# Optimization experiments

Measured on AMD Instinct MI355X. Metric: run time of the kernel, lower is better.

## Reference

```python
import jax, jax.numpy as jnp
import numpy as np

N_NODES = 1000
NODE_DIM = 40
SEQ_LEN = 12
IN_FEAT = 32
HID = 64
LAYERS = 3
GDEP = 2
TOPK = 20
TANH_ALPHA = 3.0
PROP_ALPHA = 0.05
LN_EPS = 1e-5


def setup_inputs() -> dict:
    key = jax.random.key(0)
    ks = jax.random.split(key, 20)
    s = 0.1  # weight init scale
    B = 64
    return {
        "x": jax.random.normal(ks[0], (B, N_NODES, SEQ_LEN, IN_FEAT), jnp.float32),
        # graph constructor params
        "emb1": jax.random.normal(ks[1], (N_NODES, NODE_DIM), jnp.float32) * s,
        "emb2": jax.random.normal(ks[2], (N_NODES, NODE_DIM), jnp.float32) * s,
        "lin1_w": jax.random.normal(ks[3], (NODE_DIM, NODE_DIM), jnp.float32) * s,
        "lin1_b": jnp.zeros((NODE_DIM,), jnp.float32),
        "lin2_w": jax.random.normal(ks[4], (NODE_DIM, NODE_DIM), jnp.float32) * s,
        "lin2_b": jnp.zeros((NODE_DIM,), jnp.float32),
        # LSTM (pytorch gate order i,f,g,o)
        "Wih": jax.random.normal(ks[5], (4 * HID, IN_FEAT), jnp.float32) * s,
        "Whh": jax.random.normal(ks[6], (4 * HID, HID), jnp.float32) * s,
        "bih": jnp.zeros((4 * HID,), jnp.float32),
        "bhh": jnp.zeros((4 * HID,), jnp.float32),
        # per-layer linear 64 -> seq_length
        "lin_w": jax.random.normal(ks[7], (LAYERS, SEQ_LEN, HID), jnp.float32) * s,
        "lin_b": jnp.zeros((LAYERS, SEQ_LEN), jnp.float32),
        # mixprop 1: (gdep+1)*12 -> 32
        "mp1_w": jax.random.normal(ks[8], (LAYERS, 32, (GDEP + 1) * SEQ_LEN), jnp.float32) * s,
        "mp1_b": jnp.zeros((LAYERS, 32), jnp.float32),
        # mixprop 2: (gdep+1)*32 -> node_dim
        "mp2_w": jax.random.normal(ks[9], (LAYERS, NODE_DIM, (GDEP + 1) * 32), jnp.float32) * s,
        "mp2_b": jnp.zeros((LAYERS, NODE_DIM), jnp.float32),
        # layernorm affine over (node_dim, N)
        "gamma": jnp.ones((LAYERS, NODE_DIM, N_NODES), jnp.float32),
        "beta": jnp.zeros((LAYERS, NODE_DIM, N_NODES), jnp.float32),
    }


def _graph_constructor(emb1, emb2, lin1_w, lin1_b, lin2_w, lin2_b):
    m1 = jnp.tanh(TANH_ALPHA * (emb1 @ lin1_w.T + lin1_b))
    m2 = jnp.tanh(TANH_ALPHA * (emb2 @ lin2_w.T + lin2_b))
    a = jax.nn.relu(jnp.tanh(TANH_ALPHA * (m1 @ m2.T - m2 @ m1.T)))
    _, idx = jax.lax.top_k(a, TOPK)  # keep top-k neighbors per row
    mask = jnp.zeros_like(a).at[jnp.arange(a.shape[0])[:, None], idx].set(1.0)
    return a * mask


def _lstm_last(x, Wih, Whh, bih, bhh):
    # x: (B, T, IN_FEAT) -> last hidden state (B, HID)
    B = x.shape[0]
    h0 = jnp.zeros((B, HID), x.dtype)
    c0 = jnp.zeros((B, HID), x.dtype)

    def step(carry, xt):
        h, c = carry
        g = xt @ Wih.T + h @ Whh.T + bih + bhh
        i, f, gg, o = jnp.split(g, 4, axis=-1)
        c = jax.nn.sigmoid(f) * c + jax.nn.sigmoid(i) * jnp.tanh(gg)
        h = jax.nn.sigmoid(o) * jnp.tanh(c)
        return (h, c), None

    (h, _), _ = jax.lax.scan(step, (h0, c0), jnp.swapaxes(x, 0, 1))
    return h


def _mixprop(h, adj_norm, w, b):
    # h: (B, C, N); adj_norm: (N, N) row-normalized (adj + I)
    x0 = h
    outs = [h]
    for _ in range(GDEP):
        h = PROP_ALPHA * x0 + (1.0 - PROP_ALPHA) * jnp.einsum('bcw,vw->bcv', h, adj_norm)
        outs.append(h)
    ho = jnp.concatenate(outs, axis=1)  # (B, C*(GDEP+1), N)
    return jnp.einsum('bcn,oc->bon', ho, w) + b[None, :, None]


def _layernorm(h, gamma, beta):
    # normalize over (C, N) dims
    mu = jnp.mean(h, axis=(1, 2), keepdims=True)
    var = jnp.var(h, axis=(1, 2), keepdims=True)
    return (h - mu) * jax.lax.rsqrt(var + LN_EPS) * gamma[None] + beta[None]


def reference(x, emb1, emb2, lin1_w, lin1_b, lin2_w, lin2_b,
              Wih, Whh, bih, bhh, lin_w, lin_b,
              mp1_w, mp1_b, mp2_w, mp2_b, gamma, beta):
    B, N, T, F = x.shape
    adj = _graph_constructor(emb1, emb2, lin1_w, lin1_b, lin2_w, lin2_b)
    adj = adj + jnp.eye(N, dtype=adj.dtype)
    adj_norm = adj / jnp.sum(adj, axis=1, keepdims=True)

    out = _lstm_last(x.reshape(B * N, T, F), Wih, Whh, bih, bhh)  # (B*N, 64)

    h = None
    for j in range(LAYERS):
        hj = out @ lin_w[j].T + lin_b[j]                # (B*N, 12)
        hj = hj.reshape(B, N, SEQ_LEN).transpose(0, 2, 1)  # (B, 12, N)
        hj = jax.nn.relu(_mixprop(hj, adj_norm, mp1_w[j], mp1_b[j]))
        # dropout is identity in eval mode
        hj = _mixprop(hj, adj_norm, mp2_w[j], mp2_b[j])  # (B, node_dim, N)
        h = _layernorm(hj, gamma[j], beta[j])

    return h.transpose(0, 2, 1).reshape(B, N * NODE_DIM)
```

## Files before the change

kernel.cpp:

```cpp
#include <hip/hip_runtime.h>


typedef unsigned short u16;
typedef __attribute__((ext_vector_type(8))) short bf16x8;
typedef __attribute__((ext_vector_type(4))) float fx4;

#define NB 64
#define NNODE 1000
#define TT 12
#define FF 32
#define HH 64
#define DD 40
#define TOPK_ 20
#define EPR 21

__device__ __forceinline__ float rcp_f(float x) { return __builtin_amdgcn_rcpf(x); }
__device__ __forceinline__ float tanh_f(float x) {
  return fmaf(-2.0f, rcp_f(__expf(2.0f * x) + 1.0f), 1.0f);
}
__device__ __forceinline__ unsigned int cvt_pk(float lo, float hi) {
  unsigned int r;
  asm("v_cvt_pk_bf16_f32 %0, %1, %2" : "=v"(r) : "v"(lo), "v"(hi));
  return r;
}
__device__ __forceinline__ bf16x8 cvt8(const float* p) {
  union { unsigned int u[4]; bf16x8 v; } r;
  #pragma unroll
  for (int e = 0; e < 4; e++) r.u[e] = cvt_pk(p[2 * e], p[2 * e + 1]);
  return r.v;
}
__device__ __forceinline__ bf16x8 cvt8v(float4 a, float4 b) {
  union { unsigned int u[4]; bf16x8 v; } r;
  r.u[0] = cvt_pk(a.x, a.y); r.u[1] = cvt_pk(a.z, a.w);
  r.u[2] = cvt_pk(b.x, b.y); r.u[3] = cvt_pk(b.z, b.w);
  return r.v;
}

__global__ void k_m1m2(const float* __restrict__ emb1, const float* __restrict__ emb2,
                       const float* __restrict__ w1, const float* __restrict__ b1,
                       const float* __restrict__ w2, const float* __restrict__ b2,
                       float* __restrict__ m1, float* __restrict__ m2) {
  int id = blockIdx.x * 256 + threadIdx.x;
  if (id >= 2 * NNODE * DD) return;
  int sel = id / (NNODE * DD);
  int r = id % (NNODE * DD);
  int i = r / DD, o = r % DD;
  const float* emb = sel ? emb2 : emb1;
  const float* w = sel ? w2 : w1;
  const float* bb = sel ? b2 : b1;
  float s = bb[o];
  for (int k = 0; k < DD; k++) s = fmaf(emb[i * DD + k], w[o * DD + k], s);
  (sel ? m2 : m1)[r] = tanh_f(3.0f * s);
}

__global__ void k_adj(const float* __restrict__ m1, const float* __restrict__ m2,
                      int2* __restrict__ pae) {
  int v = blockIdx.x, tid = threadIdx.x;
  __shared__ float arow[NNODE];
  __shared__ float m1v[DD], m2v[DD];
  if (tid < DD) { m1v[tid] = m1[v * DD + tid]; m2v[tid] = m2[v * DD + tid]; }
  __syncthreads();
  for (int w = tid; w < NNODE; w += 256) {
    float d1 = 0.f, d2 = 0.f;
    #pragma unroll 8
    for (int k = 0; k < DD; k++) {
      d1 = fmaf(m1v[k], m2[w * DD + k], d1);
      d2 = fmaf(m2v[k], m1[w * DD + k], d2);
    }
    arow[w] = fmaxf(tanh_f(3.0f * (d1 - d2)), 0.0f);
  }
  __syncthreads();
  if (tid >= 64) return;
  int l = tid;
  float rv[16];
  #pragma unroll
  for (int q = 0; q < 16; q++) {
    int idx = q * 64 + l;
    rv[q] = (idx < NNODE) ? arow[idx] : -2.f;
  }
  float rs = 1.f;
  float myv = 0.f; int myi = 0;
  #pragma unroll
  for (int sel = 0; sel < TOPK_; sel++) {
    float bv = rv[0]; int bi = l;
    #pragma unroll
    for (int q = 1; q < 16; q++) {
      int idx = q * 64 + l;
      if (rv[q] > bv) { bv = rv[q]; bi = idx; }
    }
    #pragma unroll
    for (int off = 1; off < 64; off <<= 1) {
      float ov = __shfl_xor(bv, off); int oi = __shfl_xor(bi, off);
      if (ov > bv || (ov == bv && oi < bi)) { bv = ov; bi = oi; }
    }
    rs += bv;
    if (l == sel + 1) { myv = bv; myi = bi; }
    #pragma unroll
    for (int q = 0; q < 16; q++)
      if (q * 64 + l == bi) rv[q] = -2.f;
  }
  float inv = rcp_f(rs);
  if (l == 0)          pae[v * EPR] = make_int2(v, __float_as_int(inv));
  else if (l <= TOPK_) pae[v * EPR + l] = make_int2(myi, __float_as_int(myv * inv));
}

__global__ __launch_bounds__(256, 2)
void k_lstm(const float* __restrict__ x, const float* __restrict__ Wih,
            const float* __restrict__ Whh, const float* __restrict__ bih,
            const float* __restrict__ bhh, const float* __restrict__ wt,
            float* __restrict__ hj) {
  __shared__ __align__(16) u16 whf[2 * 16 * 64 * 8];
  __shared__ __align__(16) u16 hsh[4][16][64];
  __shared__ float lwsh[12 * 64];
  __shared__ float lbsh[12];
  int tid = threadIdx.x, wave = tid >> 6, lane = tid & 63;
  int arow = lane & 15, kg = lane >> 4;

  for (int cc = tid; cc < 2 * 16 * 64; cc += 256) {
    int l = cc & 63, t16 = cc >> 6, ks = t16 >> 4, nt = t16 & 15;
    int row = (nt >> 2) * 64 + (l & 15) * 4 + (nt & 3);
    *(bf16x8*)&whf[cc * 8] = cvt8(Whh + row * 64 + ks * 32 + (l >> 4) * 8);
  }
  for (int i = tid; i < 768; i += 256) { int s = i >> 6, j = i & 63; lwsh[i] = wt[j * 12 + s]; }
  if (tid < 12) lbsh[tid] = wt[768 + tid];
  __syncthreads();

  bf16x8 wi[16];
  float biasv[16];
  #pragma unroll
  for (int nt = 0; nt < 16; nt++) {
    int row = (nt >> 2) * 64 + arow * 4 + (nt & 3);
    wi[nt] = cvt8(Wih + row * 32 + kg * 8);
    biasv[nt] = bih[row] + bhh[row];
  }

  int seq_base = blockIdx.x * 64 + wave * 16;
  const float* xb = x + (size_t)(seq_base + arow) * (TT * FF) + kg * 8;
  float cst[16];
  #pragma unroll
  for (int q = 0; q < 16; q++) cst[q] = 0.f;

  float4 xf0 = *(const float4*)(xb);
  float4 xf1 = *(const float4*)(xb + 4);

  auto STEP = [&](int t, bool first, float (&hq)[16]) {
    unsigned int zo = 0;
    asm volatile("" : "+v"(zo));
    bf16x8 xa = cvt8v(xf0, xf1);
    if (t < TT - 1) {
      xf0 = *(const float4*)(xb + (t + 1) * FF);
      xf1 = *(const float4*)(xb + (t + 1) * FF + 4);
    }
    fx4 acc[16];
    #pragma unroll
    for (int nt = 0; nt < 16; nt++)
      acc[nt] = (fx4){biasv[nt], biasv[nt], biasv[nt], biasv[nt]};
    #pragma unroll
    for (int nt = 0; nt < 16; nt++)
      acc[nt] = __builtin_amdgcn_mfma_f32_16x16x32_bf16(xa, wi[nt], acc[nt], 0, 0, 0);
    if (!first) {
      asm volatile("" ::: "memory");
      bf16x8 ha0 = *(const bf16x8*)&hsh[wave][arow][kg * 8];
      bf16x8 ha1 = *(const bf16x8*)&hsh[wave][arow][32 + kg * 8];
      asm volatile("" ::: "memory");
      #pragma unroll
      for (int nt = 0; nt < 16; nt++) {
        bf16x8 wb = *(const bf16x8*)&whf[(nt * 64 + lane) * 8 + zo];
        acc[nt] = __builtin_amdgcn_mfma_f32_16x16x32_bf16(ha0, wb, acc[nt], 0, 0, 0);
      }
      #pragma unroll
      for (int nt = 0; nt < 16; nt++) {
        bf16x8 wb = *(const bf16x8*)&whf[((16 + nt) * 64 + lane) * 8 + zo];
        acc[nt] = __builtin_amdgcn_mfma_f32_16x16x32_bf16(ha1, wb, acc[nt], 0, 0, 0);
      }
    }
    #pragma unroll
    for (int i = 0; i < 4; i++) {
      #pragma unroll
      for (int njt = 0; njt < 4; njt++) {
        float iv = acc[njt][i], fv = acc[njt + 4][i];
        float gv = acc[njt + 8][i], ov = acc[njt + 12][i];
        float cpv = cst[i * 4 + njt];
        float ei = __expf(-iv), ef = __expf(-fv);
        float eg = __expf(2.0f * gv), eo = __expf(-ov);
        float A = 1.0f + ef;
        float B = (1.0f + ei) * (eg + 1.0f);
        float c = fmaf(cpv, B, (eg - 1.0f) * A) * rcp_f(A * B);
        cst[i * 4 + njt] = c;
        float ec = __expf(2.0f * c);
        hq[i * 4 + njt] = (ec - 1.0f) * rcp_f((ec + 1.0f) * (1.0f + eo));
      }
    }
  };

  #pragma unroll 1
  for (int t = 0; t < TT - 1; t++) {
    float hq[16];
    STEP(t, t == 0, hq);
    #pragma unroll
    for (int i = 0; i < 4; i++) {
      unsigned int p0 = cvt_pk(hq[i * 4 + 0], hq[i * 4 + 1]);
      unsigned int p1 = cvt_pk(hq[i * 4 + 2], hq[i * 4 + 3]);
      *(uint2*)&hsh[wave][kg * 4 + i][arow * 4] = make_uint2(p0, p1);
    }
  }
  float hq[16];
  STEP(TT - 1, false, hq);

  #pragma unroll
  for (int i = 0; i < 4; i++) {
    float a[12];
    #pragma unroll
    for (int s = 0; s < 12; s++) a[s] = 0.f;
    #pragma unroll
    for (int njt = 0; njt < 4; njt++) {
      float hv = hq[i * 4 + njt];
      #pragma unroll
      for (int s = 0; s < 12; s++)
        a[s] = fmaf(hv, lwsh[s * 64 + arow * 4 + njt], a[s]);
    }
    #pragma unroll
    for (int off = 1; off < 16; off <<= 1) {
      #pragma unroll
      for (int s = 0; s < 12; s++) a[s] += __shfl_xor(a[s], off);
    }
    float outv = a[0];
    #pragma unroll
    for (int s = 1; s < 12; s++) outv = (arow == s) ? a[s] : outv;
    if (arow < 12) {
      int gseq = seq_base + kg * 4 + i;
      int bb = gseq / 1000, nn = gseq - bb * 1000;
      hj[(size_t)(bb * 12 + arow) * NNODE + nn] = outv + lbsh[arow];
    }
  }
}

__global__ void k_prep(const float* __restrict__ lw, const float* __restrict__ lb,
                       const float* __restrict__ w1, const float* __restrict__ b1,
                       const float* __restrict__ w2, const float* __restrict__ b2,
                       float* __restrict__ wt) {
  int tid = threadIdx.x;
  for (int i = tid; i < 768; i += 256) { int k = i / 12, s = i % 12; wt[i] = lw[s * 64 + k]; }
  if (tid < 12) wt[768 + tid] = lb[tid];
  for (int i = tid; i < 1152; i += 256) { int c = i / 32, o = i % 32; wt[784 + i] = w1[o * 36 + c]; }
  if (tid < 32) wt[1936 + tid] = b1[tid];
  for (int i = tid; i < 3840; i += 256) { int c = i / 40, o = i % 40; wt[1968 + i] = w2[o * 96 + c]; }
  if (tid < 40) wt[5808 + tid] = b2[tid];
}

__global__ void k_prop(const float* __restrict__ hin, const int2* __restrict__ pae,
                       float* __restrict__ ho, int C) {
  int blk = blockIdx.x;
  int b = blk / C, c = blk % C;
  __shared__ float r0[NNODE], r1[NNODE];
  int tid = threadIdx.x;
  const float* src = hin + (size_t)(b * C + c) * NNODE;
  float* dst = ho + (size_t)(b * 3 * C) * NNODE;
  for (int n = tid; n < NNODE; n += 256) {
    float vv = src[n]; r0[n] = vv; dst[(size_t)c * NNODE + n] = vv;
  }
  __syncthreads();
  for (int n = tid; n < NNODE; n += 256) {
    const int2* pa = pae + n * EPR;
    float s = 0.f;
    #pragma unroll
    for (int e = 0; e < EPR; e++) { int2 p = pa[e]; s = fmaf(__int_as_float(p.y), r0[p.x], s); }
    float h1 = 0.05f * r0[n] + 0.95f * s;
    r1[n] = h1; dst[(size_t)(C + c) * NNODE + n] = h1;
  }
  __syncthreads();
  for (int n = tid; n < NNODE; n += 256) {
    const int2* pa = pae + n * EPR;
    float s = 0.f;
    #pragma unroll
    for (int e = 0; e < EPR; e++) { int2 p = pa[e]; s = fmaf(__int_as_float(p.y), r1[p.x], s); }
    dst[(size_t)(2 * C + c) * NNODE + n] = 0.05f * r0[n] + 0.95f * s;
  }
}

template <int CIN, int COUT>
__global__ void k_proj(const float* __restrict__ hin, const float* __restrict__ wt,
                       const float* __restrict__ bb, float* __restrict__ out, int relu) {
  int id = blockIdx.x * 256 + threadIdx.x;
  int b = id / NNODE, n = id % NNODE;
  float acc[COUT];
  #pragma unroll
  for (int o = 0; o < COUT; o++) acc[o] = bb[o];
  for (int c = 0; c < CIN; c++) {
    float hv = hin[(size_t)(b * CIN + c) * NNODE + n];
    #pragma unroll
    for (int o = 0; o < COUT; o++) acc[o] = fmaf(hv, wt[c * COUT + o], acc[o]);
  }
  #pragma unroll
  for (int o = 0; o < COUT; o++) {
    float vv = acc[o];
    if (relu) vv = fmaxf(vv, 0.f);
    out[(size_t)(b * COUT + o) * NNODE + n] = vv;
  }
}

__global__ void k_lnstat(const float* __restrict__ hj2, float* __restrict__ stat) {
  int b = blockIdx.x, tid = threadIdx.x, lane = tid & 63, wave = tid >> 6;
  const float* p = hj2 + (size_t)b * DD * NNODE;
  float s = 0.f, q = 0.f;
  for (int i = tid; i < DD * NNODE; i += 256) { float vv = p[i]; s += vv; q = fmaf(vv, vv, q); }
  for (int off = 32; off; off >>= 1) { s += __shfl_down(s, off); q += __shfl_down(q, off); }
  __shared__ float ss[4], sq[4];
  if (lane == 0) { ss[wave] = s; sq[wave] = q; }
  __syncthreads();
  if (tid == 0) {
    const float invN = 1.0f / (float)(DD * NNODE);
    float S = ss[0] + ss[1] + ss[2] + ss[3];
    float Q = sq[0] + sq[1] + sq[2] + sq[3];
    float mu = S * invN;
    float var = Q * invN - mu * mu;
    stat[2 * b] = mu; stat[2 * b + 1] = __builtin_amdgcn_rsqf(var + 1e-5f);
  }
}

__global__ void k_lnapply(const float* __restrict__ hj2, const float* __restrict__ stat,
                          const float* __restrict__ gamma, const float* __restrict__ beta,
                          float* __restrict__ out) {
  int id = blockIdx.x * 256 + threadIdx.x;
  int b = id / NNODE, n = id % NNODE;
  float mu = stat[2 * b], rstd = stat[2 * b + 1];
  size_t obase = (size_t)b * (NNODE * DD) + (size_t)n * DD;
  #pragma unroll
  for (int d0 = 0; d0 < DD / 4; d0++) {
    float tt[4];
    #pragma unroll
    for (int q = 0; q < 4; q++) {
      int d = d0 * 4 + q;
      float h0 = hj2[(size_t)(b * DD + d) * NNODE + n];
      tt[q] = (h0 - mu) * rstd * gamma[d * NNODE + n] + beta[d * NNODE + n];
    }
    *(float4*)(out + obase + d0 * 4) = (float4){tt[0], tt[1], tt[2], tt[3]};
  }
}

#define OFF_M1   0
#define OFF_M2   40000
#define OFF_PAE  80000
#define OFF_HJ   4218000
#define OFF_HO1  4986000
#define OFF_O1   7290000
#define OFF_HO2  122000
#define OFF_HJ2  9338000
#define OFF_STAT 11898000
#define OFF_WT   11898128

extern "C" void kernel_launch(void* const* d_in, const int* in_sizes, int n_in,
                              void* d_out, int out_size, void* d_ws, size_t ws_size,
                              hipStream_t stream) {
  (void)in_sizes; (void)n_in; (void)out_size; (void)ws_size;
  const float* x     = (const float*)d_in[0];
  const float* emb1  = (const float*)d_in[1];
  const float* emb2  = (const float*)d_in[2];
  const float* l1w   = (const float*)d_in[3];
  const float* l1b   = (const float*)d_in[4];
  const float* l2w   = (const float*)d_in[5];
  const float* l2b   = (const float*)d_in[6];
  const float* Wih   = (const float*)d_in[7];
  const float* Whh   = (const float*)d_in[8];
  const float* bih   = (const float*)d_in[9];
  const float* bhh   = (const float*)d_in[10];
  const float* lin_w = (const float*)d_in[11];
  const float* lin_b = (const float*)d_in[12];
  const float* mp1w  = (const float*)d_in[13];
  const float* mp1b  = (const float*)d_in[14];
  const float* mp2w  = (const float*)d_in[15];
  const float* mp2b  = (const float*)d_in[16];
  const float* gamma = (const float*)d_in[17];
  const float* beta  = (const float*)d_in[18];

  float* ws   = (float*)d_ws;
  float* m1   = ws + OFF_M1;
  float* m2   = ws + OFF_M2;
  int2*  pae  = (int2*)(ws + OFF_PAE);
  float* hj   = ws + OFF_HJ;
  float* ho1  = ws + OFF_HO1;
  float* o1   = ws + OFF_O1;
  float* ho2  = ws + OFF_HO2;
  float* hj2  = ws + OFF_HJ2;
  float* stat = ws + OFF_STAT;
  float* wt   = ws + OFF_WT;

  k_m1m2<<<dim3(313), dim3(256), 0, stream>>>(emb1, emb2, l1w, l1b, l2w, l2b, m1, m2);
  k_prep<<<dim3(1), dim3(256), 0, stream>>>(lin_w + 1536, lin_b + 24, mp1w + 2304, mp1b + 64,
                                            mp2w + 7680, mp2b + 80, wt);
  k_adj<<<dim3(NNODE), dim3(256), 0, stream>>>(m1, m2, pae);
  k_lstm<<<dim3(1000), dim3(256), 0, stream>>>(x, Wih, Whh, bih, bhh, wt, hj);
  k_prop<<<dim3(64 * 12), dim3(256), 0, stream>>>(hj, pae, ho1, 12);
  k_proj<36, 32><<<dim3(250), dim3(256), 0, stream>>>(ho1, wt + 784, wt + 1936, o1, 1);
  k_prop<<<dim3(64 * 32), dim3(256), 0, stream>>>(o1, pae, ho2, 32);
  k_proj<96, 40><<<dim3(250), dim3(256), 0, stream>>>(ho2, wt + 1968, wt + 5808, hj2, 0);
  k_lnstat<<<dim3(NB), dim3(256), 0, stream>>>(hj2, stat);
  k_lnapply<<<dim3(250), dim3(256), 0, stream>>>(hj2, stat, gamma + 80000, beta + 80000,
                                                 (float*)d_out);
}
```

Measured before the change: 307.3 us.

## Vectorize loads, pad edge list to pairs, fold prep into m1m2, widen lnstat

Folds the weight-transpose prep kernel into an extra block of k_m1m2, which removes one launch. Uses float4 loads in the m1/m2 and adjacency dot products. Pads each node's edge list to 22 entries with a zero-weight dummy so k_prop can read edges as int4 pairs. Runs the layernorm stats with 1024 threads and float4 loads. The HO2 workspace offset is shifted to make room for the larger edge table, and the dummy edge adds a little work per node.

```diff
diff --git a/kernel.cpp b/kernel.cpp
--- a/kernel.cpp
+++ b/kernel.cpp
@@ -12,7 +12,7 @@
 #define HH 64
 #define DD 40
 #define TOPK_ 20
-#define EPR 21
+#define EPR2 22
 
 __device__ __forceinline__ float rcp_f(float x) { return __builtin_amdgcn_rcpf(x); }
 __device__ __forceinline__ float tanh_f(float x) {
@@ -39,17 +39,35 @@
 __global__ void k_m1m2(const float* __restrict__ emb1, const float* __restrict__ emb2,
                        const float* __restrict__ w1, const float* __restrict__ b1,
                        const float* __restrict__ w2, const float* __restrict__ b2,
-                       float* __restrict__ m1, float* __restrict__ m2) {
-  int id = blockIdx.x * 256 + threadIdx.x;
+                       float* __restrict__ m1, float* __restrict__ m2,
+                       const float* __restrict__ lw, const float* __restrict__ lb,
+                       const float* __restrict__ p1w, const float* __restrict__ p1b,
+                       const float* __restrict__ p2w, const float* __restrict__ p2b,
+                       float* __restrict__ wt) {
+  int tid = threadIdx.x;
+  if (blockIdx.x == 313) {
+    for (int i = tid; i < 768; i += 256) { int k = i / 12, s = i % 12; wt[i] = lw[s * 64 + k]; }
+    if (tid < 12) wt[768 + tid] = lb[tid];
+    for (int i = tid; i < 1152; i += 256) { int c = i / 32, o = i % 32; wt[784 + i] = p1w[o * 36 + c]; }
+    if (tid < 32) wt[1936 + tid] = p1b[tid];
+    for (int i = tid; i < 3840; i += 256) { int c = i / 40, o = i % 40; wt[1968 + i] = p2w[o * 96 + c]; }
+    if (tid < 40) wt[5808 + tid] = p2b[tid];
+    return;
+  }
+  int id = blockIdx.x * 256 + tid;
   if (id >= 2 * NNODE * DD) return;
   int sel = id / (NNODE * DD);
   int r = id % (NNODE * DD);
   int i = r / DD, o = r % DD;
-  const float* emb = sel ? emb2 : emb1;
-  const float* w = sel ? w2 : w1;
-  const float* bb = sel ? b2 : b1;
-  float s = bb[o];
-  for (int k = 0; k < DD; k++) s = fmaf(emb[i * DD + k], w[o * DD + k], s);
+  const float4* emb = (const float4*)((sel ? emb2 : emb1) + i * DD);
+  const float4* w = (const float4*)((sel ? w2 : w1) + o * DD);
+  float s = (sel ? b2 : b1)[o];
+  #pragma unroll
+  for (int k4 = 0; k4 < DD / 4; k4++) {
+    float4 a = emb[k4], b = w[k4];
+    s = fmaf(a.x, b.x, s); s = fmaf(a.y, b.y, s);
+    s = fmaf(a.z, b.z, s); s = fmaf(a.w, b.w, s);
+  }
   (sel ? m2 : m1)[r] = tanh_f(3.0f * s);
 }
 
@@ -61,11 +79,16 @@
   if (tid < DD) { m1v[tid] = m1[v * DD + tid]; m2v[tid] = m2[v * DD + tid]; }
   __syncthreads();
   for (int w = tid; w < NNODE; w += 256) {
+    const float4* m2r = (const float4*)(m2 + w * DD);
+    const float4* m1r = (const float4*)(m1 + w * DD);
     float d1 = 0.f, d2 = 0.f;
-    #pragma unroll 8
-    for (int k = 0; k < DD; k++) {
-      d1 = fmaf(m1v[k], m2[w * DD + k], d1);
-      d2 = fmaf(m2v[k], m1[w * DD + k], d2);
+    #pragma unroll
+    for (int k4 = 0; k4 < DD / 4; k4++) {
+      float4 a = m2r[k4], b = m1r[k4];
+      d1 = fmaf(m1v[k4 * 4 + 0], a.x, d1); d1 = fmaf(m1v[k4 * 4 + 1], a.y, d1);
+      d1 = fmaf(m1v[k4 * 4 + 2], a.z, d1); d1 = fmaf(m1v[k4 * 4 + 3], a.w, d1);
+      d2 = fmaf(m2v[k4 * 4 + 0], b.x, d2); d2 = fmaf(m2v[k4 * 4 + 1], b.y, d2);
+      d2 = fmaf(m2v[k4 * 4 + 2], b.z, d2); d2 = fmaf(m2v[k4 * 4 + 3], b.w, d2);
     }
     arow[w] = fmaxf(tanh_f(3.0f * (d1 - d2)), 0.0f);
   }
@@ -100,8 +123,9 @@
       if (q * 64 + l == bi) rv[q] = -2.f;
   }
   float inv = rcp_f(rs);
-  if (l == 0)          pae[v * EPR] = make_int2(v, __float_as_int(inv));
-  else if (l <= TOPK_) pae[v * EPR + l] = make_int2(myi, __float_as_int(myv * inv));
+  if (l == 0)          pae[v * EPR2] = make_int2(v, __float_as_int(inv));
+  else if (l <= TOPK_) pae[v * EPR2 + l] = make_int2(myi, __float_as_int(myv * inv));
+  else if (l == 21)    pae[v * EPR2 + 21] = make_int2(v, 0);
 }
 
 __global__ __launch_bounds__(256, 2)
@@ -235,19 +259,6 @@
   }
 }
 
-__global__ void k_prep(const float* __restrict__ lw, const float* __restrict__ lb,
-                       const float* __restrict__ w1, const float* __restrict__ b1,
-                       const float* __restrict__ w2, const float* __restrict__ b2,
-                       float* __restrict__ wt) {
-  int tid = threadIdx.x;
-  for (int i = tid; i < 768; i += 256) { int k = i / 12, s = i % 12; wt[i] = lw[s * 64 + k]; }
-  if (tid < 12) wt[768 + tid] = lb[tid];
-  for (int i = tid; i < 1152; i += 256) { int c = i / 32, o = i % 32; wt[784 + i] = w1[o * 36 + c]; }
-  if (tid < 32) wt[1936 + tid] = b1[tid];
-  for (int i = tid; i < 3840; i += 256) { int c = i / 40, o = i % 40; wt[1968 + i] = w2[o * 96 + c]; }
-  if (tid < 40) wt[5808 + tid] = b2[tid];
-}
-
 __global__ void k_prop(const float* __restrict__ hin, const int2* __restrict__ pae,
                        float* __restrict__ ho, int C) {
   int blk = blockIdx.x;
@@ -261,19 +272,27 @@
   }
   __syncthreads();
   for (int n = tid; n < NNODE; n += 256) {
-    const int2* pa = pae + n * EPR;
+    const int4* pa4 = (const int4*)(pae + (size_t)n * EPR2);
     float s = 0.f;
     #pragma unroll
-    for (int e = 0; e < EPR; e++) { int2 p = pa[e]; s = fmaf(__int_as_float(p.y), r0[p.x], s); }
+    for (int e = 0; e < EPR2 / 2; e++) {
+      int4 p = pa4[e];
+      s = fmaf(__int_as_float(p.y), r0[p.x], s);
+      s = fmaf(__int_as_float(p.w), r0[p.z], s);
+    }
     float h1 = 0.05f * r0[n] + 0.95f * s;
     r1[n] = h1; dst[(size_t)(C + c) * NNODE + n] = h1;
   }
   __syncthreads();
   for (int n = tid; n < NNODE; n += 256) {
-    const int2* pa = pae + n * EPR;
+    const int4* pa4 = (const int4*)(pae + (size_t)n * EPR2);
     float s = 0.f;
     #pragma unroll
-    for (int e = 0; e < EPR; e++) { int2 p = pa[e]; s = fmaf(__int_as_float(p.y), r1[p.x], s); }
+    for (int e = 0; e < EPR2 / 2; e++) {
+      int4 p = pa4[e];
+      s = fmaf(__int_as_float(p.y), r1[p.x], s);
+      s = fmaf(__int_as_float(p.w), r1[p.z], s);
+    }
     dst[(size_t)(2 * C + c) * NNODE + n] = 0.05f * r0[n] + 0.95f * s;
   }
 }
@@ -301,17 +320,22 @@
 
 __global__ void k_lnstat(const float* __restrict__ hj2, float* __restrict__ stat) {
   int b = blockIdx.x, tid = threadIdx.x, lane = tid & 63, wave = tid >> 6;
-  const float* p = hj2 + (size_t)b * DD * NNODE;
+  const float4* p = (const float4*)(hj2 + (size_t)b * DD * NNODE);
   float s = 0.f, q = 0.f;
-  for (int i = tid; i < DD * NNODE; i += 256) { float vv = p[i]; s += vv; q = fmaf(vv, vv, q); }
+  for (int i = tid; i < DD * NNODE / 4; i += 1024) {
+    float4 vv = p[i];
+    s += vv.x + vv.y + vv.z + vv.w;
+    q = fmaf(vv.x, vv.x, q); q = fmaf(vv.y, vv.y, q);
+    q = fmaf(vv.z, vv.z, q); q = fmaf(vv.w, vv.w, q);
+  }
   for (int off = 32; off; off >>= 1) { s += __shfl_down(s, off); q += __shfl_down(q, off); }
-  __shared__ float ss[4], sq[4];
+  __shared__ float ss[16], sq[16];
   if (lane == 0) { ss[wave] = s; sq[wave] = q; }
   __syncthreads();
   if (tid == 0) {
     const float invN = 1.0f / (float)(DD * NNODE);
-    float S = ss[0] + ss[1] + ss[2] + ss[3];
-    float Q = sq[0] + sq[1] + sq[2] + sq[3];
+    float S = 0.f, Q = 0.f;
+    for (int t = 0; t < 16; t++) { S += ss[t]; Q += sq[t]; }
     float mu = S * invN;
     float var = Q * invN - mu * mu;
     stat[2 * b] = mu; stat[2 * b + 1] = __builtin_amdgcn_rsqf(var + 1e-5f);
@@ -344,7 +368,7 @@
 #define OFF_HJ   4218000
 #define OFF_HO1  4986000
 #define OFF_O1   7290000
-#define OFF_HO2  122000
+#define OFF_HO2  124000
 #define OFF_HJ2  9338000
 #define OFF_STAT 11898000
 #define OFF_WT   11898128
@@ -385,16 +409,16 @@
   float* stat = ws + OFF_STAT;
   float* wt   = ws + OFF_WT;
 
-  k_m1m2<<<dim3(313), dim3(256), 0, stream>>>(emb1, emb2, l1w, l1b, l2w, l2b, m1, m2);
-  k_prep<<<dim3(1), dim3(256), 0, stream>>>(lin_w + 1536, lin_b + 24, mp1w + 2304, mp1b + 64,
-                                            mp2w + 7680, mp2b + 80, wt);
+  k_m1m2<<<dim3(314), dim3(256), 0, stream>>>(emb1, emb2, l1w, l1b, l2w, l2b, m1, m2,
+                                              lin_w + 1536, lin_b + 24, mp1w + 2304,
+                                              mp1b + 64, mp2w + 7680, mp2b + 80, wt);
   k_adj<<<dim3(NNODE), dim3(256), 0, stream>>>(m1, m2, pae);
   k_lstm<<<dim3(1000), dim3(256), 0, stream>>>(x, Wih, Whh, bih, bhh, wt, hj);
   k_prop<<<dim3(64 * 12), dim3(256), 0, stream>>>(hj, pae, ho1, 12);
   k_proj<36, 32><<<dim3(250), dim3(256), 0, stream>>>(ho1, wt + 784, wt + 1936, o1, 1);
   k_prop<<<dim3(64 * 32), dim3(256), 0, stream>>>(o1, pae, ho2, 32);
   k_proj<96, 40><<<dim3(250), dim3(256), 0, stream>>>(ho2, wt + 1968, wt + 5808, hj2, 0);
-  k_lnstat<<<dim3(NB), dim3(256), 0, stream>>>(hj2, stat);
+  k_lnstat<<<dim3(NB), dim3(1024), 0, stream>>>(hj2, stat);
   k_lnapply<<<dim3(250), dim3(256), 0, stream>>>(hj2, stat, gamma + 80000, beta + 80000,
                                                  (float*)d_out);
 }
```

Measured after the change: 262.2 us. 14.7% less time.
